# Performance work log

Measured on AMD Instinct MI355X. Metric: run time of the kernel, lower is better.

Reference implementation:

```python
import jax, jax.numpy as jnp
import numpy as np

B, T, N, K, d = 16, 64, 256, 8, 8
D = K * d
NEG = -9e15  # matches torch's -9000000000000000.0 sentinel


def _xavier(key, out_dim, in_dim):
    lim = float(np.sqrt(6.0 / (in_dim + out_dim)))
    return jax.random.uniform(key, (out_dim, in_dim), jnp.float32, -lim, lim)


def setup_inputs() -> dict:
    key = jax.random.key(0)
    ks = jax.random.split(key, 12)
    X = jax.random.normal(ks[0], (B, T, N, D), jnp.float32)
    STE = jax.random.normal(ks[1], (B, T, N, D), jnp.float32)
    W12 = _xavier(ks[2], D, 2 * D); b12 = jnp.zeros((D,), jnp.float32)
    W13 = _xavier(ks[3], D, 2 * D); b13 = jnp.zeros((D,), jnp.float32)
    W14 = _xavier(ks[4], D, 2 * D); b14 = jnp.zeros((D,), jnp.float32)
    W15 = _xavier(ks[5], D, D);     b15 = jnp.zeros((D,), jnp.float32)
    W16 = _xavier(ks[6], D, D);     b16 = jnp.zeros((D,), jnp.float32)
    return dict(X=X, STE=STE, W12=W12, b12=b12, W13=W13, b13=b13,
                W14=W14, b14=b14, W15=W15, b15=b15, W16=W16, b16=b16)


def reference(X, STE, W12, b12, W13, b13, W14, b14, W15, b15, W16, b16):
    gelu = lambda x: jax.nn.gelu(x, approximate=False)  # torch F.gelu default = erf
    Bv, Tv, Nv, Dv = X.shape
    H = jnp.concatenate([X, STE], axis=-1)              # [B,T,N,2D]
    # GELU-activated QKV projections, split into K heads of width d on last dim
    q = gelu(H @ W12.T + b12).reshape(Bv, Tv, Nv, K, d)
    k = gelu(H @ W13.T + b13).reshape(Bv, Tv, Nv, K, d)
    v = gelu(H @ W14.T + b14).reshape(Bv, Tv, Nv, K, d)
    # attention over time axis per (batch, vertex, head)
    attn = jnp.einsum('bqnkd,bsnkd->bnkqs', q, k) / jnp.sqrt(jnp.float32(d))
    causal = jnp.tril(jnp.ones((Tv, Tv), bool))         # [T,T]
    attn = jnp.where(causal, attn, jnp.float32(NEG))
    attn = jax.nn.softmax(attn, axis=-1)
    out = jnp.einsum('bnkqs,bsnkd->bqnkd', attn, v).reshape(Bv, Tv, Nv, Dv)
    # output MLP (dropout is identity in eval)
    return gelu(out @ W15.T + b15) @ W16.T + b16
```

## Files before the change

kernel.cpp:

```cpp
#include <hip/hip_runtime.h>
#include <hip/hip_bf16.h>

#define Bn 16
#define Tn 64
#define Nn 256
#define Kn 8
#define dn 8
#define Dn 64
#define TDn 128

typedef __bf16 bf16x8 __attribute__((ext_vector_type(8)));
typedef __bf16 bf16x4 __attribute__((ext_vector_type(4)));
typedef __bf16 bf16x2 __attribute__((ext_vector_type(2)));
typedef float  f32x4  __attribute__((ext_vector_type(4)));
typedef float  f32x16 __attribute__((ext_vector_type(16)));

#if __has_builtin(__builtin_amdgcn_exp2f)
#define EXP2F(x) __builtin_amdgcn_exp2f(x)
#else
#define EXP2F(x) exp2f(x)
#endif

#if __has_builtin(__builtin_amdgcn_rcpf)
#define RCPF(x) __builtin_amdgcn_rcpf(x)
#else
#define RCPF(x) (1.0f / (x))
#endif

__device__ __forceinline__ float geluf(float x) {
    const float x2 = x * x;
    const float v = x * fmaf(0.10294342f, x2, 2.30220920f);
    const float w = EXP2F(-fabsf(v));
    const float r = RCPF(1.0f + w);
    const float t = (1.0f - w) * r;
    return fmaf(0.5f * fabsf(x), t, 0.5f * x);
}

__device__ __forceinline__ bf16x8 bzero8() {
    bf16x8 z;
    #pragma unroll
    for (int e = 0; e < 8; ++e) z[e] = (__bf16)0.0f;
    return z;
}

__global__ void convert_weights(const float* __restrict__ W12, const float* __restrict__ W13,
                                const float* __restrict__ W14, const float* __restrict__ W15,
                                const float* __restrict__ W16, __bf16* __restrict__ ws)
{
    const int i = blockIdx.x * 256 + threadIdx.x;
    float v;
    if      (i < 8192)  v = W12[i];
    else if (i < 16384) v = W13[i - 8192];
    else if (i < 24576) v = W14[i - 16384];
    else if (i < 28672) v = W15[i - 24576];
    else                v = W16[i - 28672];
    ws[i] = (__bf16)v;
}

__global__ __launch_bounds__(256, 5)
void tam_fused(const float* __restrict__ X,
               const float* __restrict__ STE,
               const float* __restrict__ b12, const float* __restrict__ b13,
               const float* __restrict__ b14, const float* __restrict__ b15,
               const float* __restrict__ b16,
               const __bf16* __restrict__ Wb,
               float* __restrict__ Out)
{
    __shared__ __align__(16) char smem[27648];
    __bf16 (*vt)[72] = reinterpret_cast<__bf16 (*)[72]>(smem);
    __bf16 (*qs)[72] = reinterpret_cast<__bf16 (*)[72]>(smem + 9216);
    __bf16 (*ks)[72] = reinterpret_cast<__bf16 (*)[72]>(smem + 18432);

    const int bn   = blockIdx.x;
    const int b    = bn >> 8;
    const int n    = bn & 255;
    const int tid  = threadIdx.x;
    const int lane = tid & 63;
    const int wv   = __builtin_amdgcn_readfirstlane(tid >> 6);
    const int cl   = lane & 15;
    const int quad = lane >> 4;
    const int kb   = quad * 8;
    const int m0   = wv * 16;

    const __bf16* Wqkv = Wb;
    const __bf16* W15b = Wb + 24576;
    const __bf16* W16b = Wb + 28672;

    {
        bf16x8 af[4];
        {
            const int t = m0 + cl;
            const size_t rb = (((size_t)b * Tn + t) * Nn + n) * (size_t)Dn;
            const float4* Xr = reinterpret_cast<const float4*>(X + rb);
            const float4* Sr = reinterpret_cast<const float4*>(STE + rb);
            #pragma unroll
            for (int kk = 0; kk < 4; ++kk) {
                const float4* src = (kk < 2) ? Xr : Sr;
                const int fi = (kk & 1) * 8 + quad * 2;
                const float4 f0 = src[fi];
                const float4 f1 = src[fi + 1];
                bf16x8 a;
                a[0] = (__bf16)f0.x; a[1] = (__bf16)f0.y;
                a[2] = (__bf16)f0.z; a[3] = (__bf16)f0.w;
                a[4] = (__bf16)f1.x; a[5] = (__bf16)f1.y;
                a[6] = (__bf16)f1.z; a[7] = (__bf16)f1.w;
                af[kk] = a;
            }
        }

        #pragma unroll
        for (int nt = 0; nt < 12; ++nt) {
            const int n0 = nt * 16;
            f32x4 acc = {0.f, 0.f, 0.f, 0.f};
            if (nt < 8) {
                #pragma unroll
                for (int kk = 0; kk < 4; ++kk) {
                    const bf16x8 bf = *reinterpret_cast<const bf16x8*>(
                        &Wqkv[(n0 + cl) * TDn + kk * 32 + kb]);
                    acc = __builtin_amdgcn_mfma_f32_16x16x32_bf16(bf, af[kk], acc, 0, 0, 0);
                }
                if (nt < 4) {
                    const float4 bs = *reinterpret_cast<const float4*>(&b12[n0 + 4 * quad]);
                    bf16x4 pk;
                    pk[0] = (__bf16)(geluf(acc[0] + bs.x) * 0.51006951f);
                    pk[1] = (__bf16)(geluf(acc[1] + bs.y) * 0.51006951f);
                    pk[2] = (__bf16)(geluf(acc[2] + bs.z) * 0.51006951f);
                    pk[3] = (__bf16)(geluf(acc[3] + bs.w) * 0.51006951f);
                    *reinterpret_cast<bf16x4*>(&qs[m0 + cl][n0 + 4 * quad]) = pk;
                } else {
                    const float4 bs = *reinterpret_cast<const float4*>(&b13[n0 - 64 + 4 * quad]);
                    bf16x4 pk;
                    pk[0] = (__bf16)geluf(acc[0] + bs.x);
                    pk[1] = (__bf16)geluf(acc[1] + bs.y);
                    pk[2] = (__bf16)geluf(acc[2] + bs.z);
                    pk[3] = (__bf16)geluf(acc[3] + bs.w);
                    *reinterpret_cast<bf16x4*>(&ks[m0 + cl][n0 - 64 + 4 * quad]) = pk;
                }
            } else {
                #pragma unroll
                for (int kk = 0; kk < 4; ++kk) {
                    const bf16x8 bf = *reinterpret_cast<const bf16x8*>(
                        &Wqkv[(n0 + cl) * TDn + kk * 32 + kb]);
                    acc = __builtin_amdgcn_mfma_f32_16x16x32_bf16(af[kk], bf, acc, 0, 0, 0);
                }
                const float bias = b14[n0 - 128 + cl];
                bf16x4 pv;
                #pragma unroll
                for (int r = 0; r < 4; ++r) pv[r] = (__bf16)geluf(acc[r] + bias);
                *reinterpret_cast<bf16x4*>(&vt[n0 - 128 + cl][m0 + 4 * quad]) = pv;
            }
        }
    }
    __syncthreads();

    {
        const int half = lane >> 5;
        const int l31  = lane & 31;

        for (int hh = 0; hh < 2; ++hh) {
            const int hc = 8 * (2 * wv + hh);

            bf16x8 kA0 = bzero8(), kA1 = bzero8(), qB0 = bzero8(), qB1 = bzero8();
            if (half == 0) {
                kA0 = *reinterpret_cast<const bf16x8*>(&ks[ 0 + l31][hc]);
                kA1 = *reinterpret_cast<const bf16x8*>(&ks[32 + l31][hc]);
                qB0 = *reinterpret_cast<const bf16x8*>(&qs[ 0 + l31][hc]);
                qB1 = *reinterpret_cast<const bf16x8*>(&qs[32 + l31][hc]);
            }
            bf16x8 vA0 = bzero8(), vA1 = bzero8(), vA2 = bzero8(), vA3 = bzero8();
            if (l31 < 8) {
                vA0 = *reinterpret_cast<const bf16x8*>(&vt[hc + l31][ 0 + 8 * half]);
                vA1 = *reinterpret_cast<const bf16x8*>(&vt[hc + l31][16 + 8 * half]);
                vA2 = *reinterpret_cast<const bf16x8*>(&vt[hc + l31][32 + 8 * half]);
                vA3 = *reinterpret_cast<const bf16x8*>(&vt[hc + l31][48 + 8 * half]);
            }

            f32x16 zc16;
            #pragma unroll
            for (int r = 0; r < 16; ++r) zc16[r] = 0.f;

            {
                f32x16 S = __builtin_amdgcn_mfma_f32_32x32x16_bf16(kA0, qB0, zc16, 0, 0, 0);
                #pragma unroll
                for (int r = 0; r < 16; ++r) {
                    const int tk = (r & 3) + 8 * (r >> 2) + 4 * half;
                    S[r] = (tk > l31) ? -3.0e38f : S[r];
                }
                float mx = S[0];
                #pragma unroll
                for (int r = 1; r < 16; ++r) mx = fmaxf(mx, S[r]);
                mx = fmaxf(mx, __shfl_xor(mx, 32));
                float sum = 0.f;
                #pragma unroll
                for (int r = 0; r < 16; ++r) { const float p = EXP2F(S[r] - mx); S[r] = p; sum += p; }
                sum += __shfl_xor(sum, 32);

                unsigned u[8];
                #pragma unroll
                for (int i = 0; i < 8; ++i) {
                    union { __bf16 h[2]; unsigned w; } cv;
                    cv.h[0] = (__bf16)S[2 * i]; cv.h[1] = (__bf16)S[2 * i + 1];
                    u[i] = cv.w;
                }
                f32x16 O = zc16;
                #pragma unroll
                for (int c = 0; c < 2; ++c) {
                    const unsigned x0 = __shfl_xor(u[4 * c + 0], 32);
                    const unsigned x1 = __shfl_xor(u[4 * c + 1], 32);
                    const unsigned x2 = __shfl_xor(u[4 * c + 2], 32);
                    const unsigned x3 = __shfl_xor(u[4 * c + 3], 32);
                    union { unsigned w[4]; bf16x8 v; } bw;
                    bw.w[0] = half ? x2 : u[4 * c + 0];
                    bw.w[1] = half ? x3 : u[4 * c + 1];
                    bw.w[2] = half ? u[4 * c + 2] : x0;
                    bw.w[3] = half ? u[4 * c + 3] : x1;
                    O = __builtin_amdgcn_mfma_f32_32x32x16_bf16(c ? vA1 : vA0, bw.v, O, 0, 0, 0);
                }
                const float inv = RCPF(sum);
                bf16x4 ov;
                #pragma unroll
                for (int r = 0; r < 4; ++r) ov[r] = (__bf16)(O[r] * inv);
                *reinterpret_cast<bf16x4*>(&qs[l31][hc + 4 * half]) = ov;
            }

            {
                f32x16 Sa = __builtin_amdgcn_mfma_f32_32x32x16_bf16(kA0, qB1, zc16, 0, 0, 0);
                f32x16 Sb = __builtin_amdgcn_mfma_f32_32x32x16_bf16(kA1, qB1, zc16, 0, 0, 0);
                #pragma unroll
                for (int r = 0; r < 16; ++r) {
                    const int tk = (r & 3) + 8 * (r >> 2) + 4 * half;
                    Sb[r] = (tk > l31) ? -3.0e38f : Sb[r];
                }
                float mx = Sa[0];
                #pragma unroll
                for (int r = 1; r < 16; ++r) mx = fmaxf(mx, Sa[r]);
                #pragma unroll
                for (int r = 0; r < 16; ++r) mx = fmaxf(mx, Sb[r]);
                mx = fmaxf(mx, __shfl_xor(mx, 32));
                float sum = 0.f;
                #pragma unroll
                for (int r = 0; r < 16; ++r) { const float p = EXP2F(Sa[r] - mx); Sa[r] = p; sum += p; }
                #pragma unroll
                for (int r = 0; r < 16; ++r) { const float p = EXP2F(Sb[r] - mx); Sb[r] = p; sum += p; }
                sum += __shfl_xor(sum, 32);

                unsigned ua[8], ub[8];
                #pragma unroll
                for (int i = 0; i < 8; ++i) {
                    union { __bf16 h[2]; unsigned w; } cv;
                    cv.h[0] = (__bf16)Sa[2 * i]; cv.h[1] = (__bf16)Sa[2 * i + 1];
                    ua[i] = cv.w;
                }
                #pragma unroll
                for (int i = 0; i < 8; ++i) {
                    union { __bf16 h[2]; unsigned w; } cv;
                    cv.h[0] = (__bf16)Sb[2 * i]; cv.h[1] = (__bf16)Sb[2 * i + 1];
                    ub[i] = cv.w;
                }
                f32x16 O = zc16;
                #pragma unroll
                for (int c = 0; c < 4; ++c) {
                    const unsigned* uu = (c < 2) ? ua : ub;
                    const int c2 = c & 1;
                    const unsigned x0 = __shfl_xor(uu[4 * c2 + 0], 32);
                    const unsigned x1 = __shfl_xor(uu[4 * c2 + 1], 32);
                    const unsigned x2 = __shfl_xor(uu[4 * c2 + 2], 32);
                    const unsigned x3 = __shfl_xor(uu[4 * c2 + 3], 32);
                    union { unsigned w[4]; bf16x8 v; } bw;
                    bw.w[0] = half ? x2 : uu[4 * c2 + 0];
                    bw.w[1] = half ? x3 : uu[4 * c2 + 1];
                    bw.w[2] = half ? uu[4 * c2 + 2] : x0;
                    bw.w[3] = half ? uu[4 * c2 + 3] : x1;
                    const bf16x8 vA = (c == 0) ? vA0 : (c == 1) ? vA1 : (c == 2) ? vA2 : vA3;
                    O = __builtin_amdgcn_mfma_f32_32x32x16_bf16(vA, bw.v, O, 0, 0, 0);
                }
                const float inv = RCPF(sum);
                bf16x4 ov;
                #pragma unroll
                for (int r = 0; r < 4; ++r) ov[r] = (__bf16)(O[r] * inv);
                *reinterpret_cast<bf16x4*>(&qs[32 + l31][hc + 4 * half]) = ov;
            }
        }
    }
    __syncthreads();

    {
        const bf16x8 h0 = *reinterpret_cast<const bf16x8*>(&qs[m0 + cl][kb]);
        const bf16x8 h1 = *reinterpret_cast<const bf16x8*>(&qs[m0 + cl][32 + kb]);
        #pragma unroll
        for (int nt = 0; nt < 4; ++nt) {
            const int n0 = nt * 16;
            f32x4 acc = {0.f, 0.f, 0.f, 0.f};
            const bf16x8 w0 = *reinterpret_cast<const bf16x8*>(&W15b[(n0 + cl) * Dn + kb]);
            acc = __builtin_amdgcn_mfma_f32_16x16x32_bf16(w0, h0, acc, 0, 0, 0);
            const bf16x8 w1 = *reinterpret_cast<const bf16x8*>(&W15b[(n0 + cl) * Dn + 32 + kb]);
            acc = __builtin_amdgcn_mfma_f32_16x16x32_bf16(w1, h1, acc, 0, 0, 0);
            const float4 bs = *reinterpret_cast<const float4*>(&b15[n0 + 4 * quad]);
            bf16x4 pk;
            pk[0] = (__bf16)geluf(acc[0] + bs.x);
            pk[1] = (__bf16)geluf(acc[1] + bs.y);
            pk[2] = (__bf16)geluf(acc[2] + bs.z);
            pk[3] = (__bf16)geluf(acc[3] + bs.w);
            *reinterpret_cast<bf16x4*>(&ks[m0 + cl][n0 + 4 * quad]) = pk;
        }
    }

    {
        const bf16x8 h0 = *reinterpret_cast<const bf16x8*>(&ks[m0 + cl][kb]);
        const bf16x8 h1 = *reinterpret_cast<const bf16x8*>(&ks[m0 + cl][32 + kb]);
        const size_t ob = (((size_t)(b * Tn + m0 + cl)) * Nn + n) * (size_t)Dn;
        #pragma unroll
        for (int nt = 0; nt < 4; ++nt) {
            const int n0 = nt * 16;
            f32x4 acc = {0.f, 0.f, 0.f, 0.f};
            const bf16x8 w0 = *reinterpret_cast<const bf16x8*>(&W16b[(n0 + cl) * Dn + kb]);
            acc = __builtin_amdgcn_mfma_f32_16x16x32_bf16(w0, h0, acc, 0, 0, 0);
            const bf16x8 w1 = *reinterpret_cast<const bf16x8*>(&W16b[(n0 + cl) * Dn + 32 + kb]);
            acc = __builtin_amdgcn_mfma_f32_16x16x32_bf16(w1, h1, acc, 0, 0, 0);
            const float4 bs = *reinterpret_cast<const float4*>(&b16[n0 + 4 * quad]);
            float4 ov;
            ov.x = acc[0] + bs.x;
            ov.y = acc[1] + bs.y;
            ov.z = acc[2] + bs.z;
            ov.w = acc[3] + bs.w;
            *reinterpret_cast<float4*>(&Out[ob + n0 + 4 * quad]) = ov;
        }
    }
}

extern "C" void kernel_launch(void* const* d_in, const int* in_sizes, int n_in,
                              void* d_out, int out_size, void* d_ws, size_t ws_size,
                              hipStream_t stream)
{
    (void)in_sizes; (void)n_in; (void)out_size; (void)ws_size;
    const float* X   = (const float*)d_in[0];
    const float* STE = (const float*)d_in[1];
    const float* W12 = (const float*)d_in[2];
    const float* b12 = (const float*)d_in[3];
    const float* W13 = (const float*)d_in[4];
    const float* b13 = (const float*)d_in[5];
    const float* W14 = (const float*)d_in[6];
    const float* b14 = (const float*)d_in[7];
    const float* W15 = (const float*)d_in[8];
    const float* b15 = (const float*)d_in[9];
    const float* W16 = (const float*)d_in[10];
    const float* b16 = (const float*)d_in[11];
    float* Out = (float*)d_out;
    __bf16* ws = (__bf16*)d_ws;

    hipLaunchKernelGGL(convert_weights, dim3(128), dim3(256), 0, stream,
                       W12, W13, W14, W15, W16, ws);
    hipLaunchKernelGGL(tam_fused, dim3(Bn * Nn), dim3(256), 0, stream,
                       X, STE, b12, b13, b14, b15, b16, ws, Out);
}
```

Measured before the change: 281.9 us.

## Process two vertices per block to reuse weight loads and interleave MFMA chains

Each block now handles two adjacent vertices (n, n+1) instead of one. Grid size is halved and shared memory doubled to hold per-vertex Q/K/V buffers. Weight fragments are loaded once and applied to both vertices, and the two independent MFMA and softmax chains are interleaved to expose instruction-level parallelism. The reads of the two adjacent vertex rows also become more contiguous. In exchange, register pressure and LDS use go up, and launch bounds drop from 5 to 2 blocks per CU, which lowers occupancy.

New measurement: 253.1 us. 1.11x faster.

```diff
diff --git a/kernel.cpp b/kernel.cpp
--- a/kernel.cpp
+++ b/kernel.cpp
@@ -11,7 +11,6 @@
 
 typedef __bf16 bf16x8 __attribute__((ext_vector_type(8)));
 typedef __bf16 bf16x4 __attribute__((ext_vector_type(4)));
-typedef __bf16 bf16x2 __attribute__((ext_vector_type(2)));
 typedef float  f32x4  __attribute__((ext_vector_type(4)));
 typedef float  f32x16 __attribute__((ext_vector_type(16)));
 
@@ -41,6 +40,15 @@
     #pragma unroll
     for (int e = 0; e < 8; ++e) z[e] = (__bf16)0.0f;
     return z;
+}
+
+__device__ __forceinline__ bf16x8 pack8(float4 f0, float4 f1) {
+    bf16x8 a;
+    a[0] = (__bf16)f0.x; a[1] = (__bf16)f0.y;
+    a[2] = (__bf16)f0.z; a[3] = (__bf16)f0.w;
+    a[4] = (__bf16)f1.x; a[5] = (__bf16)f1.y;
+    a[6] = (__bf16)f1.z; a[7] = (__bf16)f1.w;
+    return a;
 }
 
 __global__ void convert_weights(const float* __restrict__ W12, const float* __restrict__ W13,
@@ -57,7 +65,7 @@
     ws[i] = (__bf16)v;
 }
 
-__global__ __launch_bounds__(256, 5)
+__global__ __launch_bounds__(256, 2)
 void tam_fused(const float* __restrict__ X,
                const float* __restrict__ STE,
                const float* __restrict__ b12, const float* __restrict__ b13,
@@ -66,14 +74,17 @@
                const __bf16* __restrict__ Wb,
                float* __restrict__ Out)
 {
-    __shared__ __align__(16) char smem[27648];
-    __bf16 (*vt)[72] = reinterpret_cast<__bf16 (*)[72]>(smem);
-    __bf16 (*qs)[72] = reinterpret_cast<__bf16 (*)[72]>(smem + 9216);
-    __bf16 (*ks)[72] = reinterpret_cast<__bf16 (*)[72]>(smem + 18432);
+    __shared__ __align__(16) char smem[55296];
+    __bf16 (*vtP[2])[72] = { reinterpret_cast<__bf16 (*)[72]>(smem),
+                             reinterpret_cast<__bf16 (*)[72]>(smem + 27648) };
+    __bf16 (*qsP[2])[72] = { reinterpret_cast<__bf16 (*)[72]>(smem + 9216),
+                             reinterpret_cast<__bf16 (*)[72]>(smem + 27648 + 9216) };
+    __bf16 (*ksP[2])[72] = { reinterpret_cast<__bf16 (*)[72]>(smem + 18432),
+                             reinterpret_cast<__bf16 (*)[72]>(smem + 27648 + 18432) };
 
     const int bn   = blockIdx.x;
-    const int b    = bn >> 8;
-    const int n    = bn & 255;
+    const int b    = bn >> 7;
+    const int n0   = (bn & 127) * 2;
     const int tid  = threadIdx.x;
     const int lane = tid & 63;
     const int wv   = __builtin_amdgcn_readfirstlane(tid >> 6);
@@ -87,67 +98,79 @@
     const __bf16* W16b = Wb + 28672;
 
     {
-        bf16x8 af[4];
+        bf16x8 af[2][4];
         {
             const int t = m0 + cl;
-            const size_t rb = (((size_t)b * Tn + t) * Nn + n) * (size_t)Dn;
-            const float4* Xr = reinterpret_cast<const float4*>(X + rb);
-            const float4* Sr = reinterpret_cast<const float4*>(STE + rb);
-            #pragma unroll
-            for (int kk = 0; kk < 4; ++kk) {
-                const float4* src = (kk < 2) ? Xr : Sr;
-                const int fi = (kk & 1) * 8 + quad * 2;
-                const float4 f0 = src[fi];
-                const float4 f1 = src[fi + 1];
-                bf16x8 a;
-                a[0] = (__bf16)f0.x; a[1] = (__bf16)f0.y;
-                a[2] = (__bf16)f0.z; a[3] = (__bf16)f0.w;
-                a[4] = (__bf16)f1.x; a[5] = (__bf16)f1.y;
-                a[6] = (__bf16)f1.z; a[7] = (__bf16)f1.w;
-                af[kk] = a;
+            const size_t rb = (((size_t)b * Tn + t) * Nn + n0) * (size_t)Dn;
+            #pragma unroll
+            for (int c = 0; c < 2; ++c) {
+                const float4* Xr = reinterpret_cast<const float4*>(X + rb + c * Dn);
+                const float4* Sr = reinterpret_cast<const float4*>(STE + rb + c * Dn);
+                const int fi = quad * 2;
+                const float4 x0 = Xr[fi], x1 = Xr[fi + 1];
+                const float4 x2 = Xr[8 + fi], x3 = Xr[8 + fi + 1];
+                const float4 s0 = Sr[fi], s1 = Sr[fi + 1];
+                const float4 s2 = Sr[8 + fi], s3 = Sr[8 + fi + 1];
+                af[c][0] = pack8(x0, x1);
+                af[c][1] = pack8(x2, x3);
+                af[c][2] = pack8(s0, s1);
+                af[c][3] = pack8(s2, s3);
             }
         }
 
         #pragma unroll
         for (int nt = 0; nt < 12; ++nt) {
-            const int n0 = nt * 16;
-            f32x4 acc = {0.f, 0.f, 0.f, 0.f};
+            const int nf = nt * 16;
+            bf16x8 wq[4];
+            #pragma unroll
+            for (int kk = 0; kk < 4; ++kk)
+                wq[kk] = *reinterpret_cast<const bf16x8*>(&Wqkv[(nf + cl) * TDn + kk * 32 + kb]);
+            f32x4 acc[2] = { {0.f, 0.f, 0.f, 0.f}, {0.f, 0.f, 0.f, 0.f} };
             if (nt < 8) {
                 #pragma unroll
                 for (int kk = 0; kk < 4; ++kk) {
-                    const bf16x8 bf = *reinterpret_cast<const bf16x8*>(
-                        &Wqkv[(n0 + cl) * TDn + kk * 32 + kb]);
-                    acc = __builtin_amdgcn_mfma_f32_16x16x32_bf16(bf, af[kk], acc, 0, 0, 0);
+                    #pragma unroll
+                    for (int c = 0; c < 2; ++c)
+                        acc[c] = __builtin_amdgcn_mfma_f32_16x16x32_bf16(wq[kk], af[c][kk], acc[c], 0, 0, 0);
                 }
                 if (nt < 4) {
-                    const float4 bs = *reinterpret_cast<const float4*>(&b12[n0 + 4 * quad]);
-                    bf16x4 pk;
-                    pk[0] = (__bf16)(geluf(acc[0] + bs.x) * 0.51006951f);
-                    pk[1] = (__bf16)(geluf(acc[1] + bs.y) * 0.51006951f);
-                    pk[2] = (__bf16)(geluf(acc[2] + bs.z) * 0.51006951f);
-                    pk[3] = (__bf16)(geluf(acc[3] + bs.w) * 0.51006951f);
-                    *reinterpret_cast<bf16x4*>(&qs[m0 + cl][n0 + 4 * quad]) = pk;
+                    const float4 bs = *reinterpret_cast<const float4*>(&b12[nf + 4 * quad]);
+                    #pragma unroll
+                    for (int c = 0; c < 2; ++c) {
+                        bf16x4 pk;
+                        pk[0] = (__bf16)(geluf(acc[c][0] + bs.x) * 0.51006951f);
+                        pk[1] = (__bf16)(geluf(acc[c][1] + bs.y) * 0.51006951f);
+                        pk[2] = (__bf16)(geluf(acc[c][2] + bs.z) * 0.51006951f);
+                        pk[3] = (__bf16)(geluf(acc[c][3] + bs.w) * 0.51006951f);
+                        *reinterpret_cast<bf16x4*>(&qsP[c][m0 + cl][nf + 4 * quad]) = pk;
+                    }
                 } else {
-                    const float4 bs = *reinterpret_cast<const float4*>(&b13[n0 - 64 + 4 * quad]);
-                    bf16x4 pk;
-                    pk[0] = (__bf16)geluf(acc[0] + bs.x);
-                    pk[1] = (__bf16)geluf(acc[1] + bs.y);
-                    pk[2] = (__bf16)geluf(acc[2] + bs.z);
-                    pk[3] = (__bf16)geluf(acc[3] + bs.w);
-                    *reinterpret_cast<bf16x4*>(&ks[m0 + cl][n0 - 64 + 4 * quad]) = pk;
+                    const float4 bs = *reinterpret_cast<const float4*>(&b13[nf - 64 + 4 * quad]);
+                    #pragma unroll
+                    for (int c = 0; c < 2; ++c) {
+                        bf16x4 pk;
+                        pk[0] = (__bf16)geluf(acc[c][0] + bs.x);
+                        pk[1] = (__bf16)geluf(acc[c][1] + bs.y);
+                        pk[2] = (__bf16)geluf(acc[c][2] + bs.z);
+                        pk[3] = (__bf16)geluf(acc[c][3] + bs.w);
+                        *reinterpret_cast<bf16x4*>(&ksP[c][m0 + cl][nf - 64 + 4 * quad]) = pk;
+                    }
                 }
             } else {
                 #pragma unroll
                 for (int kk = 0; kk < 4; ++kk) {
-                    const bf16x8 bf = *reinterpret_cast<const bf16x8*>(
-                        &Wqkv[(n0 + cl) * TDn + kk * 32 + kb]);
-                    acc = __builtin_amdgcn_mfma_f32_16x16x32_bf16(af[kk], bf, acc, 0, 0, 0);
-                }
-                const float bias = b14[n0 - 128 + cl];
-                bf16x4 pv;
-                #pragma unroll
-                for (int r = 0; r < 4; ++r) pv[r] = (__bf16)geluf(acc[r] + bias);
-                *reinterpret_cast<bf16x4*>(&vt[n0 - 128 + cl][m0 + 4 * quad]) = pv;
+                    #pragma unroll
+                    for (int c = 0; c < 2; ++c)
+                        acc[c] = __builtin_amdgcn_mfma_f32_16x16x32_bf16(af[c][kk], wq[kk], acc[c], 0, 0, 0);
+                }
+                const float vbias = b14[nf - 128 + cl];
+                #pragma unroll
+                for (int c = 0; c < 2; ++c) {
+                    bf16x4 pv;
+                    #pragma unroll
+                    for (int r = 0; r < 4; ++r) pv[r] = (__bf16)geluf(acc[c][r] + vbias);
+                    *reinterpret_cast<bf16x4*>(&vtP[c][nf - 128 + cl][m0 + 4 * quad]) = pv;
+                }
             }
         }
     }
@@ -160,19 +183,21 @@
         for (int hh = 0; hh < 2; ++hh) {
             const int hc = 8 * (2 * wv + hh);
 
-            bf16x8 kA0 = bzero8(), kA1 = bzero8(), qB0 = bzero8(), qB1 = bzero8();
-            if (half == 0) {
-                kA0 = *reinterpret_cast<const bf16x8*>(&ks[ 0 + l31][hc]);
-                kA1 = *reinterpret_cast<const bf16x8*>(&ks[32 + l31][hc]);
-                qB0 = *reinterpret_cast<const bf16x8*>(&qs[ 0 + l31][hc]);
-                qB1 = *reinterpret_cast<const bf16x8*>(&qs[32 + l31][hc]);
-            }
-            bf16x8 vA0 = bzero8(), vA1 = bzero8(), vA2 = bzero8(), vA3 = bzero8();
-            if (l31 < 8) {
-                vA0 = *reinterpret_cast<const bf16x8*>(&vt[hc + l31][ 0 + 8 * half]);
-                vA1 = *reinterpret_cast<const bf16x8*>(&vt[hc + l31][16 + 8 * half]);
-                vA2 = *reinterpret_cast<const bf16x8*>(&vt[hc + l31][32 + 8 * half]);
-                vA3 = *reinterpret_cast<const bf16x8*>(&vt[hc + l31][48 + 8 * half]);
+            bf16x8 kA0[2], kA1[2], qB0[2], qB1[2], vA0[2], vA1[2];
+            #pragma unroll
+            for (int c = 0; c < 2; ++c) {
+                kA0[c] = bzero8(); kA1[c] = bzero8(); qB0[c] = bzero8(); qB1[c] = bzero8();
+                vA0[c] = bzero8(); vA1[c] = bzero8();
+                if (half == 0) {
+                    kA0[c] = *reinterpret_cast<const bf16x8*>(&ksP[c][ 0 + l31][hc]);
+                    kA1[c] = *reinterpret_cast<const bf16x8*>(&ksP[c][32 + l31][hc]);
+                    qB0[c] = *reinterpret_cast<const bf16x8*>(&qsP[c][ 0 + l31][hc]);
+                    qB1[c] = *reinterpret_cast<const bf16x8*>(&qsP[c][32 + l31][hc]);
+                }
+                if (l31 < 8) {
+                    vA0[c] = *reinterpret_cast<const bf16x8*>(&vtP[c][hc + l31][ 0 + 8 * half]);
+                    vA1[c] = *reinterpret_cast<const bf16x8*>(&vtP[c][hc + l31][16 + 8 * half]);
+                }
             }
 
             f32x16 zc16;
@@ -180,150 +205,225 @@
             for (int r = 0; r < 16; ++r) zc16[r] = 0.f;
 
             {
-                f32x16 S = __builtin_amdgcn_mfma_f32_32x32x16_bf16(kA0, qB0, zc16, 0, 0, 0);
+                f32x16 S[2];
+                #pragma unroll
+                for (int c = 0; c < 2; ++c)
+                    S[c] = __builtin_amdgcn_mfma_f32_32x32x16_bf16(kA0[c], qB0[c], zc16, 0, 0, 0);
                 #pragma unroll
                 for (int r = 0; r < 16; ++r) {
                     const int tk = (r & 3) + 8 * (r >> 2) + 4 * half;
-                    S[r] = (tk > l31) ? -3.0e38f : S[r];
-                }
-                float mx = S[0];
-                #pragma unroll
-                for (int r = 1; r < 16; ++r) mx = fmaxf(mx, S[r]);
-                mx = fmaxf(mx, __shfl_xor(mx, 32));
-                float sum = 0.f;
-                #pragma unroll
-                for (int r = 0; r < 16; ++r) { const float p = EXP2F(S[r] - mx); S[r] = p; sum += p; }
-                sum += __shfl_xor(sum, 32);
-
-                unsigned u[8];
+                    #pragma unroll
+                    for (int c = 0; c < 2; ++c) S[c][r] = (tk > l31) ? -3.0e38f : S[c][r];
+                }
+                float mx[2] = { S[0][0], S[1][0] };
+                #pragma unroll
+                for (int r = 1; r < 16; ++r) {
+                    #pragma unroll
+                    for (int c = 0; c < 2; ++c) mx[c] = fmaxf(mx[c], S[c][r]);
+                }
+                #pragma unroll
+                for (int c = 0; c < 2; ++c) mx[c] = fmaxf(mx[c], __shfl_xor(mx[c], 32));
+                float sum[2] = { 0.f, 0.f };
+                #pragma unroll
+                for (int r = 0; r < 16; ++r) {
+                    #pragma unroll
+                    for (int c = 0; c < 2; ++c) {
+                        const float p = EXP2F(S[c][r] - mx[c]);
+                        S[c][r] = p; sum[c] += p;
+                    }
+                }
+                #pragma unroll
+                for (int c = 0; c < 2; ++c) sum[c] += __shfl_xor(sum[c], 32);
+
+                unsigned u[2][8];
                 #pragma unroll
                 for (int i = 0; i < 8; ++i) {
-                    union { __bf16 h[2]; unsigned w; } cv;
-                    cv.h[0] = (__bf16)S[2 * i]; cv.h[1] = (__bf16)S[2 * i + 1];
-                    u[i] = cv.w;
-                }
-                f32x16 O = zc16;
+                    #pragma unroll
+                    for (int c = 0; c < 2; ++c) {
+                        union { __bf16 h[2]; unsigned w; } cv;
+                        cv.h[0] = (__bf16)S[c][2 * i]; cv.h[1] = (__bf16)S[c][2 * i + 1];
+                        u[c][i] = cv.w;
+                    }
+                }
+                f32x16 O[2] = { zc16, zc16 };
+                #pragma unroll
+                for (int ch = 0; ch < 2; ++ch) {
+                    #pragma unroll
+                    for (int c = 0; c < 2; ++c) {
+                        const unsigned x0 = __shfl_xor(u[c][4 * ch + 0], 32);
+                        const unsigned x1 = __shfl_xor(u[c][4 * ch + 1], 32);
+                        const unsigned x2 = __shfl_xor(u[c][4 * ch + 2], 32);
+                        const unsigned x3 = __shfl_xor(u[c][4 * ch + 3], 32);
+                        union { unsigned w[4]; bf16x8 v; } bw;
+                        bw.w[0] = half ? x2 : u[c][4 * ch + 0];
+                        bw.w[1] = half ? x3 : u[c][4 * ch + 1];
+                        bw.w[2] = half ? u[c][4 * ch + 2] : x0;
+                        bw.w[3] = half ? u[c][4 * ch + 3] : x1;
+                        O[c] = __builtin_amdgcn_mfma_f32_32x32x16_bf16(ch ? vA1[c] : vA0[c],
+                                                                       bw.v, O[c], 0, 0, 0);
+                    }
+                }
                 #pragma unroll
                 for (int c = 0; c < 2; ++c) {
-                    const unsigned x0 = __shfl_xor(u[4 * c + 0], 32);
-                    const unsigned x1 = __shfl_xor(u[4 * c + 1], 32);
-                    const unsigned x2 = __shfl_xor(u[4 * c + 2], 32);
-                    const unsigned x3 = __shfl_xor(u[4 * c + 3], 32);
-                    union { unsigned w[4]; bf16x8 v; } bw;
-                    bw.w[0] = half ? x2 : u[4 * c + 0];
-                    bw.w[1] = half ? x3 : u[4 * c + 1];
-                    bw.w[2] = half ? u[4 * c + 2] : x0;
-                    bw.w[3] = half ? u[4 * c + 3] : x1;
-                    O = __builtin_amdgcn_mfma_f32_32x32x16_bf16(c ? vA1 : vA0, bw.v, O, 0, 0, 0);
-                }
-                const float inv = RCPF(sum);
-                bf16x4 ov;
-                #pragma unroll
-                for (int r = 0; r < 4; ++r) ov[r] = (__bf16)(O[r] * inv);
-                *reinterpret_cast<bf16x4*>(&qs[l31][hc + 4 * half]) = ov;
+                    const float inv = RCPF(sum[c]);
+                    bf16x4 ov;
+                    #pragma unroll
+                    for (int r = 0; r < 4; ++r) ov[r] = (__bf16)(O[c][r] * inv);
+                    *reinterpret_cast<bf16x4*>(&qsP[c][l31][hc + 4 * half]) = ov;
+                }
             }
 
             {
-                f32x16 Sa = __builtin_amdgcn_mfma_f32_32x32x16_bf16(kA0, qB1, zc16, 0, 0, 0);
-                f32x16 Sb = __builtin_amdgcn_mfma_f32_32x32x16_bf16(kA1, qB1, zc16, 0, 0, 0);
+                bf16x8 vA2[2], vA3[2];
+                #pragma unroll
+                for (int c = 0; c < 2; ++c) {
+                    vA2[c] = bzero8(); vA3[c] = bzero8();
+                    if (l31 < 8) {
+                        vA2[c] = *reinterpret_cast<const bf16x8*>(&vtP[c][hc + l31][32 + 8 * half]);
+                        vA3[c] = *reinterpret_cast<const bf16x8*>(&vtP[c][hc + l31][48 + 8 * half]);
+                    }
+                }
+                f32x16 Sa[2], Sb[2];
+                #pragma unroll
+                for (int c = 0; c < 2; ++c) {
+                    Sa[c] = __builtin_amdgcn_mfma_f32_32x32x16_bf16(kA0[c], qB1[c], zc16, 0, 0, 0);
+                    Sb[c] = __builtin_amdgcn_mfma_f32_32x32x16_bf16(kA1[c], qB1[c], zc16, 0, 0, 0);
+                }
                 #pragma unroll
                 for (int r = 0; r < 16; ++r) {
                     const int tk = (r & 3) + 8 * (r >> 2) + 4 * half;
-                    Sb[r] = (tk > l31) ? -3.0e38f : Sb[r];
-                }
-                float mx = Sa[0];
-                #pragma unroll
-                for (int r = 1; r < 16; ++r) mx = fmaxf(mx, Sa[r]);
-                #pragma unroll
-                for (int r = 0; r < 16; ++r) mx = fmaxf(mx, Sb[r]);
-                mx = fmaxf(mx, __shfl_xor(mx, 32));
-                float sum = 0.f;
-                #pragma unroll
-                for (int r = 0; r < 16; ++r) { const float p = EXP2F(Sa[r] - mx); Sa[r] = p; sum += p; }
-                #pragma unroll
-                for (int r = 0; r < 16; ++r) { const float p = EXP2F(Sb[r] - mx); Sb[r] = p; sum += p; }
-                sum += __shfl_xor(sum, 32);
-
-                unsigned ua[8], ub[8];
+                    #pragma unroll
+                    for (int c = 0; c < 2; ++c) Sb[c][r] = (tk > l31) ? -3.0e38f : Sb[c][r];
+                }
+                float mx[2] = { Sa[0][0], Sa[1][0] };
+                #pragma unroll
+                for (int r = 1; r < 16; ++r) {
+                    #pragma unroll
+                    for (int c = 0; c < 2; ++c) mx[c] = fmaxf(mx[c], Sa[c][r]);
+                }
+                #pragma unroll
+                for (int r = 0; r < 16; ++r) {
+                    #pragma unroll
+                    for (int c = 0; c < 2; ++c) mx[c] = fmaxf(mx[c], Sb[c][r]);
+                }
+                #pragma unroll
+                for (int c = 0; c < 2; ++c) mx[c] = fmaxf(mx[c], __shfl_xor(mx[c], 32));
+                float sum[2] = { 0.f, 0.f };
+                #pragma unroll
+                for (int r = 0; r < 16; ++r) {
+                    #pragma unroll
+                    for (int c = 0; c < 2; ++c) {
+                        const float p = EXP2F(Sa[c][r] - mx[c]); Sa[c][r] = p; sum[c] += p;
+                    }
+                }
+                #pragma unroll
+                for (int r = 0; r < 16; ++r) {
+                    #pragma unroll
+                    for (int c = 0; c < 2; ++c) {
+                        const float p = EXP2F(Sb[c][r] - mx[c]); Sb[c][r] = p; sum[c] += p;
+                    }
+                }
+                #pragma unroll
+                for (int c = 0; c < 2; ++c) sum[c] += __shfl_xor(sum[c], 32);
+
+                unsigned ua[2][8], ub[2][8];
                 #pragma unroll
                 for (int i = 0; i < 8; ++i) {
-                    union { __bf16 h[2]; unsigned w; } cv;
-                    cv.h[0] = (__bf16)Sa[2 * i]; cv.h[1] = (__bf16)Sa[2 * i + 1];
-                    ua[i] = cv.w;
-                }
-                #pragma unroll
-                for (int i = 0; i < 8; ++i) {
-                    union { __bf16 h[2]; unsigned w; } cv;
-                    cv.h[0] = (__bf16)Sb[2 * i]; cv.h[1] = (__bf16)Sb[2 * i + 1];
-                    ub[i] = cv.w;
-                }
-                f32x16 O = zc16;
-                #pragma unroll
-                for (int c = 0; c < 4; ++c) {
-                    const unsigned* uu = (c < 2) ? ua : ub;
-                    const int c2 = c & 1;
-                    const unsigned x0 = __shfl_xor(uu[4 * c2 + 0], 32);
-                    const unsigned x1 = __shfl_xor(uu[4 * c2 + 1], 32);
-                    const unsigned x2 = __shfl_xor(uu[4 * c2 + 2], 32);
-                    const unsigned x3 = __shfl_xor(uu[4 * c2 + 3], 32);
-                    union { unsigned w[4]; bf16x8 v; } bw;
-                    bw.w[0] = half ? x2 : uu[4 * c2 + 0];
-                    bw.w[1] = half ? x3 : uu[4 * c2 + 1];
-                    bw.w[2] = half ? uu[4 * c2 + 2] : x0;
-                    bw.w[3] = half ? uu[4 * c2 + 3] : x1;
-                    const bf16x8 vA = (c == 0) ? vA0 : (c == 1) ? vA1 : (c == 2) ? vA2 : vA3;
-                    O = __builtin_amdgcn_mfma_f32_32x32x16_bf16(vA, bw.v, O, 0, 0, 0);
-                }
-                const float inv = RCPF(sum);
-                bf16x4 ov;
-                #pragma unroll
-                for (int r = 0; r < 4; ++r) ov[r] = (__bf16)(O[r] * inv);
-                *reinterpret_cast<bf16x4*>(&qs[32 + l31][hc + 4 * half]) = ov;
+                    #pragma unroll
+                    for (int c = 0; c < 2; ++c) {
+                        union { __bf16 h[2]; unsigned w; } cv;
+                        cv.h[0] = (__bf16)Sa[c][2 * i]; cv.h[1] = (__bf16)Sa[c][2 * i + 1];
+                        ua[c][i] = cv.w;
+                        union { __bf16 h[2]; unsigned w; } cw;
+                        cw.h[0] = (__bf16)Sb[c][2 * i]; cw.h[1] = (__bf16)Sb[c][2 * i + 1];
+                        ub[c][i] = cw.w;
+                    }
+                }
+                f32x16 O[2] = { zc16, zc16 };
+                #pragma unroll
+                for (int ch = 0; ch < 4; ++ch) {
+                    const int c2 = ch & 1;
+                    #pragma unroll
+                    for (int c = 0; c < 2; ++c) {
+                        const unsigned* uu = (ch < 2) ? ua[c] : ub[c];
+                        const unsigned x0 = __shfl_xor(uu[4 * c2 + 0], 32);
+                        const unsigned x1 = __shfl_xor(uu[4 * c2 + 1], 32);
+                        const unsigned x2 = __shfl_xor(uu[4 * c2 + 2], 32);
+                        const unsigned x3 = __shfl_xor(uu[4 * c2 + 3], 32);
+                        union { unsigned w[4]; bf16x8 v; } bw;
+                        bw.w[0] = half ? x2 : uu[4 * c2 + 0];
+                        bw.w[1] = half ? x3 : uu[4 * c2 + 1];
+                        bw.w[2] = half ? uu[4 * c2 + 2] : x0;
+                        bw.w[3] = half ? uu[4 * c2 + 3] : x1;
+                        const bf16x8 vA = (ch == 0) ? vA0[c] : (ch == 1) ? vA1[c]
+                                        : (ch == 2) ? vA2[c] : vA3[c];
+                        O[c] = __builtin_amdgcn_mfma_f32_32x32x16_bf16(vA, bw.v, O[c], 0, 0, 0);
+                    }
+                }
+                #pragma unroll
+                for (int c = 0; c < 2; ++c) {
+                    const float inv = RCPF(sum[c]);
+                    bf16x4 ov;
+                    #pragma unroll
+                    for (int r = 0; r < 4; ++r) ov[r] = (__bf16)(O[c][r] * inv);
+                    *reinterpret_cast<bf16x4*>(&qsP[c][32 + l31][hc + 4 * half]) = ov;
+                }
             }
         }
     }
     __syncthreads();
 
     {
-        const bf16x8 h0 = *reinterpret_cast<const bf16x8*>(&qs[m0 + cl][kb]);
-        const bf16x8 h1 = *reinterpret_cast<const bf16x8*>(&qs[m0 + cl][32 + kb]);
+        bf16x8 h0[2], h1[2];
+        #pragma unroll
+        for (int c = 0; c < 2; ++c) {
+            h0[c] = *reinterpret_cast<const bf16x8*>(&qsP[c][m0 + cl][kb]);
+            h1[c] = *reinterpret_cast<const bf16x8*>(&qsP[c][m0 + cl][32 + kb]);
+        }
         #pragma unroll
         for (int nt = 0; nt < 4; ++nt) {
-            const int n0 = nt * 16;
-            f32x4 acc = {0.f, 0.f, 0.f, 0.f};
-            const bf16x8 w0 = *reinterpret_cast<const bf16x8*>(&W15b[(n0 + cl) * Dn + kb]);
-            acc = __builtin_amdgcn_mfma_f32_16x16x32_bf16(w0, h0, acc, 0, 0, 0);
-            const bf16x8 w1 = *reinterpret_cast<const bf16x8*>(&W15b[(n0 + cl) * Dn + 32 + kb]);
-            acc = __builtin_amdgcn_mfma_f32_16x16x32_bf16(w1, h1, acc, 0, 0, 0);
-            const float4 bs = *reinterpret_cast<const float4*>(&b15[n0 + 4 * quad]);
-            bf16x4 pk;
-            pk[0] = (__bf16)geluf(acc[0] + bs.x);
-            pk[1] = (__bf16)geluf(acc[1] + bs.y);
-            pk[2] = (__bf16)geluf(acc[2] + bs.z);
-            pk[3] = (__bf16)geluf(acc[3] + bs.w);
-            *reinterpret_cast<bf16x4*>(&ks[m0 + cl][n0 + 4 * quad]) = pk;
-        }
-    }
-
-    {
-        const bf16x8 h0 = *reinterpret_cast<const bf16x8*>(&ks[m0 + cl][kb]);
-        const bf16x8 h1 = *reinterpret_cast<const bf16x8*>(&ks[m0 + cl][32 + kb]);
-        const size_t ob = (((size_t)(b * Tn + m0 + cl)) * Nn + n) * (size_t)Dn;
+            const int nf = nt * 16;
+            const bf16x8 w0 = *reinterpret_cast<const bf16x8*>(&W15b[(nf + cl) * Dn + kb]);
+            const bf16x8 w1 = *reinterpret_cast<const bf16x8*>(&W15b[(nf + cl) * Dn + 32 + kb]);
+            const float4 bs = *reinterpret_cast<const float4*>(&b15[nf + 4 * quad]);
+            #pragma unroll
+            for (int c = 0; c < 2; ++c) {
+                f32x4 acc = {0.f, 0.f, 0.f, 0.f};
+                acc = __builtin_amdgcn_mfma_f32_16x16x32_bf16(w0, h0[c], acc, 0, 0, 0);
+                acc = __builtin_amdgcn_mfma_f32_16x16x32_bf16(w1, h1[c], acc, 0, 0, 0);
+                bf16x4 pk;
+                pk[0] = (__bf16)geluf(acc[0] + bs.x);
+                pk[1] = (__bf16)geluf(acc[1] + bs.y);
+                pk[2] = (__bf16)geluf(acc[2] + bs.z);
+                pk[3] = (__bf16)geluf(acc[3] + bs.w);
+                *reinterpret_cast<bf16x4*>(&ksP[c][m0 + cl][nf + 4 * quad]) = pk;
+            }
+        }
+        bf16x8 g0[2], g1[2];
+        #pragma unroll
+        for (int c = 0; c < 2; ++c) {
+            g0[c] = *reinterpret_cast<const bf16x8*>(&ksP[c][m0 + cl][kb]);
+            g1[c] = *reinterpret_cast<const bf16x8*>(&ksP[c][m0 + cl][32 + kb]);
+        }
+        const size_t ob = (((size_t)(b * Tn + m0 + cl)) * Nn + n0) * (size_t)Dn;
         #pragma unroll
         for (int nt = 0; nt < 4; ++nt) {
-            const int n0 = nt * 16;
-            f32x4 acc = {0.f, 0.f, 0.f, 0.f};
-            const bf16x8 w0 = *reinterpret_cast<const bf16x8*>(&W16b[(n0 + cl) * Dn + kb]);
-            acc = __builtin_amdgcn_mfma_f32_16x16x32_bf16(w0, h0, acc, 0, 0, 0);
-            const bf16x8 w1 = *reinterpret_cast<const bf16x8*>(&W16b[(n0 + cl) * Dn + 32 + kb]);
-            acc = __builtin_amdgcn_mfma_f32_16x16x32_bf16(w1, h1, acc, 0, 0, 0);
-            const float4 bs = *reinterpret_cast<const float4*>(&b16[n0 + 4 * quad]);
-            float4 ov;
-            ov.x = acc[0] + bs.x;
-            ov.y = acc[1] + bs.y;
-            ov.z = acc[2] + bs.z;
-            ov.w = acc[3] + bs.w;
-            *reinterpret_cast<float4*>(&Out[ob + n0 + 4 * quad]) = ov;
+            const int nf = nt * 16;
+            const bf16x8 w0 = *reinterpret_cast<const bf16x8*>(&W16b[(nf + cl) * Dn + kb]);
+            const bf16x8 w1 = *reinterpret_cast<const bf16x8*>(&W16b[(nf + cl) * Dn + 32 + kb]);
+            const float4 bs = *reinterpret_cast<const float4*>(&b16[nf + 4 * quad]);
+            #pragma unroll
+            for (int c = 0; c < 2; ++c) {
+                f32x4 acc = {0.f, 0.f, 0.f, 0.f};
+                acc = __builtin_amdgcn_mfma_f32_16x16x32_bf16(w0, g0[c], acc, 0, 0, 0);
+                acc = __builtin_amdgcn_mfma_f32_16x16x32_bf16(w1, g1[c], acc, 0, 0, 0);
+                float4 ov;
+                ov.x = acc[0] + bs.x;
+                ov.y = acc[1] + bs.y;
+                ov.z = acc[2] + bs.z;
+                ov.w = acc[3] + bs.w;
+                *reinterpret_cast<float4*>(&Out[ob + (size_t)c * Dn + nf + 4 * quad]) = ov;
+            }
         }
     }
 }
@@ -350,6 +450,6 @@
 
     hipLaunchKernelGGL(convert_weights, dim3(128), dim3(256), 0, stream,
                        W12, W13, W14, W15, W16, ws);
-    hipLaunchKernelGGL(tam_fused, dim3(Bn * Nn), dim3(256), 0, stream,
+    hipLaunchKernelGGL(tam_fused, dim3(Bn * Nn / 2), dim3(256), 0, stream,
                        X, STE, b12, b13, b14, b15, b16, ws, Out);
 }
```
